# Performance work log

Hardware: AMD Instinct MI355X
Metric: run time of the kernel (lower is better)

The kernel has to match this reference:

```python
import jax, jax.numpy as jnp
import numpy as np

SAMPLE_RATE = 256
WIN = 64          # round(256*250/1000)
HOP = 32          # round(256*125/1000)
HIDDEN = 512
PER_CHAN = 8
MAX_CH = 64
_EEG_BANDS = ((0.5, 4.0), (4.0, 8.0), (8.0, 13.0), (13.0, 30.0), (30.0, 100.0))

_FREQS = np.fft.rfftfreq(WIN, d=1.0 / SAMPLE_RATE)
_BAND_MASKS = [np.logical_and(_FREQS >= lo, _FREQS < hi) for (lo, hi) in _EEG_BANDS]


def _sinusoidal_1d(n, dim, dtype=jnp.float32):
    pos = jnp.arange(n, dtype=jnp.float32)[:, None]
    half = dim // 2
    div = jnp.exp(jnp.arange(half, dtype=jnp.float32) * (-np.log(10000.0) / half))
    ang = pos * div[None, :]
    pe = jnp.zeros((n, dim), dtype=jnp.float32)
    pe = pe.at[:, 0::2].set(jnp.sin(ang))
    pe = pe.at[:, 1::2].set(jnp.cos(ang))
    return pe.astype(dtype)


def setup_inputs() -> dict:
    key = jax.random.key(0)
    k = jax.random.split(key, 5)
    B, T, C = 8, 65536, 64
    return {
        "signal": jax.random.normal(k[0], (B, T, C), dtype=jnp.float32),
        "chan_w": 0.02 * jax.random.normal(k[1], (MAX_CH, 7, PER_CHAN), dtype=jnp.float32),
        "chan_b": 0.02 * jax.random.normal(k[2], (MAX_CH, PER_CHAN), dtype=jnp.float32),
        "mix_w": 0.02 * jax.random.normal(k[3], (HIDDEN, MAX_CH * PER_CHAN), dtype=jnp.float32),
        "marker": 0.02 * jax.random.normal(k[4], (HIDDEN,), dtype=jnp.float32),
    }


def reference(signal, chan_w, chan_b, mix_w, marker):
    B, T, C = signal.shape  # C == MAX_CH, no padding/mask branch
    Tw = (T - WIN) // HOP + 1
    idx = jnp.arange(Tw)[:, None] * HOP + jnp.arange(WIN)[None, :]
    x = jnp.transpose(signal[:, idx, :], (0, 1, 3, 2))
    # spectral features
    mag = jnp.abs(jnp.fft.rfft(x, axis=-1))
    band_feats = jnp.stack(
        [mag[..., m].mean(axis=-1) if m.any() else jnp.zeros(mag.shape[:-1], mag.dtype)
         for m in _BAND_MASKS],
        axis=-1,
    )  # (B, Tw, C, 5)
    mean = x.mean(axis=-1, keepdims=True)
    std = jnp.std(x, axis=-1, ddof=1, keepdims=True)  # torch std is unbiased
    feats = jnp.concatenate([band_feats, mean, std], axis=-1)  # (B, Tw, C, 7)
    # per-channel projection + bias
    emb = jnp.einsum("btcf,cfp->btcp", feats, chan_w) + chan_b[None, None]
    flat = emb.reshape(B, Tw, MAX_CH * PER_CHAN)
    z = flat @ mix_w.T  # (B, Tw, HIDDEN)
    z = z + _sinusoidal_1d(Tw, HIDDEN, z.dtype)[None]
    mk = jnp.broadcast_to(marker[None, None, :], (B, 1, HIDDEN))
    return jnp.concatenate([mk, z], axis=1)  # (B, 1+Tw, HIDDEN)
```

## Files before the change

### kernel.cpp

```cpp
#include <hip/hip_runtime.h>
#include <stdint.h>

#define TW_N 2047
#define BATCH 8
#define T_LEN 65536
#define NCH 64
#define HID 512
#define NWIN (BATCH * TW_N)

typedef unsigned short ushortT;

__device__ __forceinline__ ushortT f2b(float f) {
  union { float f; uint32_t i; } v; v.f = f;
  uint32_t r = v.i + 0x7fffu + ((v.i >> 16) & 1u);
  return (ushortT)(r >> 16);
}
__device__ __forceinline__ uint32_t pk2(float lo, float hi) {
  return (uint32_t)f2b(lo) | ((uint32_t)f2b(hi) << 16);
}

__device__ __forceinline__ void gload_lds16(const void* g, void* l) {
  __builtin_amdgcn_global_load_lds(
      (const __attribute__((address_space(1))) uint32_t*)g,
      (__attribute__((address_space(3))) uint32_t*)l, 16, 0, 0);
}

constexpr float CQ[17] = {
  1.0f, 0.9951847267f, 0.9807852804f, 0.9569403357f, 0.9238795325f,
  0.8819212643f, 0.8314696123f, 0.7730104534f, 0.7071067812f, 0.6343932842f,
  0.5555702330f, 0.4713967368f, 0.3826834324f, 0.2902846773f, 0.1950903220f,
  0.0980171403f, 0.0f };
constexpr float cos64(int m) {
  m &= 63;
  return (m <= 16) ? CQ[m] : (m < 32) ? -CQ[32 - m] : (m < 48) ? -CQ[m - 32] : CQ[64 - m];
}
constexpr float sin64(int m) { return cos64(m - 16); }
struct TwTab { float c[24][32]; float s[24][32]; };
constexpr TwTab make_tab() {
  TwTab t{};
  for (int i = 0; i < 24; ++i)
    for (int j = 0; j < 32; ++j) {
      int m = ((i + 1) * j) & 63;
      t.c[i][j] = cos64(m);
      t.s[i][j] = sin64(m);
    }
  return t;
}
constexpr TwTab TT = make_tab();

__device__ ushortT Bpack[HID * HID];

__global__ __launch_bounds__(256) void prep_kernel(
    const float* __restrict__ marker, const float* __restrict__ Bw,
    float* __restrict__ out)
{
  const int gid = blockIdx.x * 256 + threadIdx.x;
  if (blockIdx.x < 16) {
    out[(size_t)(gid >> 9) * (2048 * 512) + (gid & 511)] = marker[gid & 511];
  } else {
    const int i = (gid - 4096) * 8;
    const float4 f0 = *(const float4*)(Bw + i);
    const float4 f1 = *(const float4*)(Bw + i + 4);
    uint4 u;
    u.x = pk2(f0.x, f0.y); u.y = pk2(f0.z, f0.w);
    u.z = pk2(f1.x, f1.y); u.w = pk2(f1.z, f1.w);
    *(uint4*)(Bpack + i) = u;
  }
}

#define WPB 8
#define SROWS 288

__global__ __launch_bounds__(512) void feat_embed_kernel(
    const float* __restrict__ sig, const float* __restrict__ chw,
    const float* __restrict__ chb, ushortT* __restrict__ flatB)
{
  __shared__ float xs[SROWS * NCH];
  const int tid = threadIdx.x;
  const int tile = blockIdx.x;
  const int b = blockIdx.y;
  const int t0 = tile * (WPB * 32);

  const float* sgb = sig + (size_t)b * T_LEN * NCH;
#pragma unroll
  for (int k = 0; k < 9; ++k) {
    const int idx = tid + k * 512;
    int row = t0 + (idx >> 4);
    row = row < T_LEN ? row : T_LEN - 1;
    gload_lds16(sgb + (size_t)row * NCH + (idx & 15) * 4, (char*)xs + (size_t)idx * 16);
  }
  __syncthreads();

  const int wv = tid >> 6;
  const int c = tid & 63;
  int wl = tile * WPB + wv;
  wl = wl < TW_N ? wl : TW_N - 1;
  const int lv = wl - tile * WPB;
  const float* base = xs + lv * (32 * NCH) + c;

  float e[32], o[32];
  float sum = 0.f, sumsq = 0.f;
#pragma unroll
  for (int t = 0; t < 32; ++t) {
    const float a = base[t * 64];
    const float d = base[(t + 32) * 64];
    e[t] = a + d; o[t] = a - d;
    sum += e[t];
    sumsq = fmaf(a, a, fmaf(d, d, sumsq));
  }

  float b1 = 0.f, b2 = 0.f, b3 = 0.f, b4 = 0.f;
#pragma unroll
  for (int i = 0; i < 24; ++i) {
    const int k = i + 1;
    float re = 0.f, im = 0.f;
#pragma unroll
    for (int t = 0; t < 32; ++t) {
      const float v = (k & 1) ? o[t] : e[t];
      re = fmaf(v, TT.c[i][t], re);
      im = fmaf(v, TT.s[i][t], im);
    }
    const float mag = sqrtf(fmaf(re, re, im * im));
    if (k == 1) b1 += mag;
    else if (k < 4) b2 += mag;
    else if (k < 8) b3 += mag;
    else b4 += mag;
  }

  const float mean = sum * (1.f / 64.f);
  const float var = (sumsq - sum * sum * (1.f / 64.f)) * (1.f / 63.f);
  const float sd = sqrtf(fmaxf(var, 0.f));

  float feats[7];
  feats[0] = 0.f;
  feats[1] = b1;
  feats[2] = b2 * 0.5f;
  feats[3] = b3 * 0.25f;
  feats[4] = b4 * (1.f / 17.f);
  feats[5] = mean;
  feats[6] = sd;

  const float* wr = chw + c * 56;
  float emb[8];
#pragma unroll
  for (int p = 0; p < 8; ++p) emb[p] = chb[c * 8 + p];
#pragma unroll
  for (int f = 1; f < 7; ++f) {
    const float fv = feats[f];
#pragma unroll
    for (int p = 0; p < 8; ++p) emb[p] = fmaf(fv, wr[f * 8 + p], emb[p]);
  }

  uint32_t pka[4];
#pragma unroll
  for (int q = 0; q < 4; ++q) pka[q] = pk2(emb[2 * q], emb[2 * q + 1]);
  const int w = b * TW_N + wl;
  *(uint4*)(flatB + (size_t)w * HID + c * 8) = make_uint4(pka[0], pka[1], pka[2], pka[3]);
}

typedef __attribute__((ext_vector_type(8))) short short8;
typedef __attribute__((ext_vector_type(4))) float f32x4;

__global__ __launch_bounds__(256) void mix_gemm_kernel(
    const ushortT* __restrict__ A,
    float* __restrict__ out)
{
  __shared__ ushortT As[2][128 * 32];
  __shared__ ushortT Bs[2][128 * 32];

  const int tid = threadIdx.x;
  const int lane = tid & 63;
  const int wv = tid >> 6;
  const int wm = wv >> 1, wn = wv & 1;
  const int fr = lane & 15;
  const int fq = lane >> 4;

  const int n0 = blockIdx.x * 128;
  const int m0 = blockIdx.y * 128;

  const int srow = tid >> 2;
  const int sko = (tid & 3) * 8;

  f32x4 acc[4][4];
#pragma unroll
  for (int i = 0; i < 4; ++i)
#pragma unroll
    for (int j = 0; j < 4; ++j) acc[i][j] = (f32x4){0.f, 0.f, 0.f, 0.f};

  int am0 = m0 + srow;       am0 = am0 < NWIN ? am0 : NWIN - 1;
  int am1 = m0 + 64 + srow;  am1 = am1 < NWIN ? am1 : NWIN - 1;
  const ushortT* ga0 = A + (size_t)am0 * HID + sko;
  const ushortT* ga1 = A + (size_t)am1 * HID + sko;
  const ushortT* gb0 = Bpack + (size_t)(n0 + srow) * HID + sko;
  const ushortT* gb1 = Bpack + (size_t)(n0 + 64 + srow) * HID + sko;

#define STAGE(buf, kt) do {                                                    \
    const int ko_ = (kt) * 32;                                                 \
    gload_lds16(ga0 + ko_, (char*)&As[buf][0] + tid * 16);                     \
    gload_lds16(ga1 + ko_, (char*)&As[buf][0] + 4096 + tid * 16);              \
    gload_lds16(gb0 + ko_, (char*)&Bs[buf][0] + tid * 16);                     \
    gload_lds16(gb1 + ko_, (char*)&Bs[buf][0] + 4096 + tid * 16);              \
  } while (0)

  STAGE(0, 0);

  for (int kt = 0; kt < 16; ++kt) {
    const int cur = kt & 1;
    if (kt < 15) {
      STAGE(cur ^ 1, kt + 1);
      asm volatile("s_waitcnt vmcnt(4)\n\ts_barrier" ::: "memory");
    } else {
      asm volatile("s_waitcnt vmcnt(0)\n\ts_barrier" ::: "memory");
    }

    short8 af[4], bf[4];
#pragma unroll
    for (int mt = 0; mt < 4; ++mt)
      af[mt] = *(const short8*)&As[cur][(wm * 64 + mt * 16 + fr) * 32 + fq * 8];
#pragma unroll
    for (int nt = 0; nt < 4; ++nt)
      bf[nt] = *(const short8*)&Bs[cur][(wn * 64 + nt * 16 + fr) * 32 + fq * 8];
#pragma unroll
    for (int mt = 0; mt < 4; ++mt)
#pragma unroll
      for (int nt = 0; nt < 4; ++nt)
        acc[mt][nt] = __builtin_amdgcn_mfma_f32_16x16x32_bf16(af[mt], bf[nt], acc[mt][nt], 0, 0, 0);

    asm volatile("s_barrier" ::: "memory");
  }
#undef STAGE

#pragma unroll
  for (int nt = 0; nt < 4; ++nt) {
    const int ng = n0 + wn * 64 + nt * 16 + fr;
    const float dv = __expf(-0.03597789208f * (float)(ng >> 1));
    const bool odd = (ng & 1);
#pragma unroll
    for (int mt = 0; mt < 4; ++mt) {
#pragma unroll
      for (int r = 0; r < 4; ++r) {
        const int mg = m0 + wm * 64 + mt * 16 + fq * 4 + r;
        if (mg < NWIN) {
          const int bb = mg / TW_N;
          const int tw = mg - bb * TW_N;
          const float ang = (float)tw * dv;
          const float pev = odd ? __cosf(ang) : __sinf(ang);
          out[((size_t)(bb * 2048 + 1 + tw)) * HID + ng] = acc[mt][nt][r] + pev;
        }
      }
    }
  }
}

extern "C" void kernel_launch(void* const* d_in, const int* in_sizes, int n_in,
                              void* d_out, int out_size, void* d_ws, size_t ws_size,
                              hipStream_t stream)
{
  const float* sig = (const float*)d_in[0];
  const float* chw = (const float*)d_in[1];
  const float* chb = (const float*)d_in[2];
  const float* mxw = (const float*)d_in[3];
  const float* mkr = (const float*)d_in[4];
  float* out = (float*)d_out;

  ushortT* flatB = (ushortT*)d_ws;

  hipLaunchKernelGGL(prep_kernel, dim3(144), dim3(256), 0, stream, mkr, mxw, out);
  hipLaunchKernelGGL(feat_embed_kernel, dim3(256, 8), dim3(512), 0, stream, sig, chw, chb, flatB);
  hipLaunchKernelGGL(mix_gemm_kernel, dim3(4, 128), dim3(256), 0, stream, flatB, out);
}
```

Measured before the change: 266.2 us.

## Stream feature windows per wave with register sliding reuse; triple-buffer GEMM LDS

The feature kernel no longer stages signal tiles through LDS. Each wave now handles a run of 8 consecutive windows for one batch and slides a 64-sample window through registers, reusing the overlapping half and loading the next half-window one iteration ahead. This drops the LDS traffic, the barrier and the redundant halo loads, but launches far fewer waves and runs a serial per-wave loop, so latency hiding may suffer. Separately, the mix GEMM moves from double to triple LDS buffering with a deeper vmcnt wait, so global loads are issued two k-steps ahead.

```diff
diff --git a/kernel.cpp b/kernel.cpp
--- a/kernel.cpp
+++ b/kernel.cpp
@@ -68,94 +68,92 @@
   }
 }
 
-#define WPB 8
-#define SROWS 288
-
-__global__ __launch_bounds__(512) void feat_embed_kernel(
+__global__ __launch_bounds__(256) void feat_embed_kernel(
     const float* __restrict__ sig, const float* __restrict__ chw,
     const float* __restrict__ chb, ushortT* __restrict__ flatB)
 {
-  __shared__ float xs[SROWS * NCH];
   const int tid = threadIdx.x;
-  const int tile = blockIdx.x;
-  const int b = blockIdx.y;
-  const int t0 = tile * (WPB * 32);
-
-  const float* sgb = sig + (size_t)b * T_LEN * NCH;
-#pragma unroll
-  for (int k = 0; k < 9; ++k) {
-    const int idx = tid + k * 512;
-    int row = t0 + (idx >> 4);
-    row = row < T_LEN ? row : T_LEN - 1;
-    gload_lds16(sgb + (size_t)row * NCH + (idx & 15) * 4, (char*)xs + (size_t)idx * 16);
-  }
-  __syncthreads();
-
-  const int wv = tid >> 6;
   const int c = tid & 63;
-  int wl = tile * WPB + wv;
-  wl = wl < TW_N ? wl : TW_N - 1;
-  const int lv = wl - tile * WPB;
-  const float* base = xs + lv * (32 * NCH) + c;
-
-  float e[32], o[32];
-  float sum = 0.f, sumsq = 0.f;
-#pragma unroll
-  for (int t = 0; t < 32; ++t) {
-    const float a = base[t * 64];
-    const float d = base[(t + 32) * 64];
-    e[t] = a + d; o[t] = a - d;
-    sum += e[t];
-    sumsq = fmaf(a, a, fmaf(d, d, sumsq));
-  }
-
-  float b1 = 0.f, b2 = 0.f, b3 = 0.f, b4 = 0.f;
-#pragma unroll
-  for (int i = 0; i < 24; ++i) {
-    const int k = i + 1;
-    float re = 0.f, im = 0.f;
+  const int gw = blockIdx.x * 4 + (tid >> 6);
+  const int b = gw >> 8;
+  const int run = gw & 255;
+  const int tw0 = run * 8;
+  const int nw = (tw0 + 8 <= TW_N) ? 8 : (TW_N - tw0);
+  const float* sg = sig + ((size_t)b * T_LEN + (size_t)tw0 * 32) * NCH + c;
+  const float* wr = chw + c * 56;
+
+  float A[32], Bh[32], O[32], R[32];
+#pragma unroll
+  for (int t = 0; t < 32; ++t) A[t] = sg[t * 64];
+#pragma unroll
+  for (int t = 0; t < 32; ++t) Bh[t] = sg[(t + 32) * 64];
+
+#pragma unroll 1
+  for (int l = 0; l < nw; ++l) {
+    {
+      int hrow = (tw0 + l + 2) * 32;
+      hrow = hrow < (T_LEN - 32) ? hrow : (T_LEN - 32);
+      const float* pn = sig + ((size_t)b * T_LEN + hrow) * NCH + c;
+#pragma unroll
+      for (int t = 0; t < 32; ++t) R[t] = pn[t * 64];
+    }
+
+    float sum = 0.f, sumsq = 0.f;
 #pragma unroll
     for (int t = 0; t < 32; ++t) {
-      const float v = (k & 1) ? o[t] : e[t];
-      re = fmaf(v, TT.c[i][t], re);
-      im = fmaf(v, TT.s[i][t], im);
-    }
-    const float mag = sqrtf(fmaf(re, re, im * im));
-    if (k == 1) b1 += mag;
-    else if (k < 4) b2 += mag;
-    else if (k < 8) b3 += mag;
-    else b4 += mag;
-  }
-
-  const float mean = sum * (1.f / 64.f);
-  const float var = (sumsq - sum * sum * (1.f / 64.f)) * (1.f / 63.f);
-  const float sd = sqrtf(fmaxf(var, 0.f));
-
-  float feats[7];
-  feats[0] = 0.f;
-  feats[1] = b1;
-  feats[2] = b2 * 0.5f;
-  feats[3] = b3 * 0.25f;
-  feats[4] = b4 * (1.f / 17.f);
-  feats[5] = mean;
-  feats[6] = sd;
-
-  const float* wr = chw + c * 56;
-  float emb[8];
-#pragma unroll
-  for (int p = 0; p < 8; ++p) emb[p] = chb[c * 8 + p];
-#pragma unroll
-  for (int f = 1; f < 7; ++f) {
-    const float fv = feats[f];
-#pragma unroll
-    for (int p = 0; p < 8; ++p) emb[p] = fmaf(fv, wr[f * 8 + p], emb[p]);
-  }
-
-  uint32_t pka[4];
-#pragma unroll
-  for (int q = 0; q < 4; ++q) pka[q] = pk2(emb[2 * q], emb[2 * q + 1]);
-  const int w = b * TW_N + wl;
-  *(uint4*)(flatB + (size_t)w * HID + c * 8) = make_uint4(pka[0], pka[1], pka[2], pka[3]);
+      O[t] = A[t] - Bh[t];
+      A[t] = A[t] + Bh[t];
+      sum += A[t];
+      sumsq = fmaf(A[t], A[t], fmaf(O[t], O[t], sumsq));
+    }
+
+    float b1 = 0.f, b2 = 0.f, b3 = 0.f, b4 = 0.f;
+#pragma unroll
+    for (int i = 0; i < 24; ++i) {
+      const int k = i + 1;
+      float re = 0.f, im = 0.f;
+#pragma unroll
+      for (int t = 0; t < 32; ++t) {
+        const float v = (k & 1) ? O[t] : A[t];
+        re = fmaf(v, TT.c[i][t], re);
+        im = fmaf(v, TT.s[i][t], im);
+      }
+      const float mag = __builtin_amdgcn_sqrtf(fmaf(re, re, im * im));
+      if (k == 1) b1 += mag;
+      else if (k < 4) b2 += mag;
+      else if (k < 8) b3 += mag;
+      else b4 += mag;
+    }
+
+    const float mean = sum * (1.f / 64.f);
+    const float var = (sumsq * 0.5f - sum * sum * (1.f / 64.f)) * (1.f / 63.f);
+    const float sd = __builtin_amdgcn_sqrtf(fmaxf(var, 0.f));
+
+    const float f1 = b1, f2 = b2 * 0.5f, f3 = b3 * 0.25f, f4 = b4 * (1.f / 17.f);
+    float emb[8];
+#pragma unroll
+    for (int p = 0; p < 8; ++p) emb[p] = chb[c * 8 + p];
+#pragma unroll
+    for (int p = 0; p < 8; ++p) {
+      float e = emb[p];
+      e = fmaf(f1, wr[8 + p], e);
+      e = fmaf(f2, wr[16 + p], e);
+      e = fmaf(f3, wr[24 + p], e);
+      e = fmaf(f4, wr[32 + p], e);
+      e = fmaf(mean, wr[40 + p], e);
+      e = fmaf(sd, wr[48 + p], e);
+      emb[p] = e;
+    }
+
+    uint32_t pka[4];
+#pragma unroll
+    for (int q = 0; q < 4; ++q) pka[q] = pk2(emb[2 * q], emb[2 * q + 1]);
+    const int w = b * TW_N + tw0 + l;
+    *(uint4*)(flatB + (size_t)w * HID + c * 8) = make_uint4(pka[0], pka[1], pka[2], pka[3]);
+
+#pragma unroll
+    for (int t = 0; t < 32; ++t) { A[t] = Bh[t]; Bh[t] = R[t]; }
+  }
 }
 
 typedef __attribute__((ext_vector_type(8))) short short8;
@@ -165,8 +163,8 @@
     const ushortT* __restrict__ A,
     float* __restrict__ out)
 {
-  __shared__ ushortT As[2][128 * 32];
-  __shared__ ushortT Bs[2][128 * 32];
+  __shared__ ushortT As[3][128 * 32];
+  __shared__ ushortT Bs[3][128 * 32];
 
   const int tid = threadIdx.x;
   const int lane = tid & 63;
@@ -203,11 +201,14 @@
   } while (0)
 
   STAGE(0, 0);
-
+  STAGE(1, 1);
+
+  int c0 = 0, c1 = 1, c2 = 2;
   for (int kt = 0; kt < 16; ++kt) {
-    const int cur = kt & 1;
-    if (kt < 15) {
-      STAGE(cur ^ 1, kt + 1);
+    if (kt < 14) {
+      STAGE(c2, kt + 2);
+      asm volatile("s_waitcnt vmcnt(8)\n\ts_barrier" ::: "memory");
+    } else if (kt == 14) {
       asm volatile("s_waitcnt vmcnt(4)\n\ts_barrier" ::: "memory");
     } else {
       asm volatile("s_waitcnt vmcnt(0)\n\ts_barrier" ::: "memory");
@@ -216,10 +217,10 @@
     short8 af[4], bf[4];
 #pragma unroll
     for (int mt = 0; mt < 4; ++mt)
-      af[mt] = *(const short8*)&As[cur][(wm * 64 + mt * 16 + fr) * 32 + fq * 8];
+      af[mt] = *(const short8*)&As[c0][(wm * 64 + mt * 16 + fr) * 32 + fq * 8];
 #pragma unroll
     for (int nt = 0; nt < 4; ++nt)
-      bf[nt] = *(const short8*)&Bs[cur][(wn * 64 + nt * 16 + fr) * 32 + fq * 8];
+      bf[nt] = *(const short8*)&Bs[c0][(wn * 64 + nt * 16 + fr) * 32 + fq * 8];
 #pragma unroll
     for (int mt = 0; mt < 4; ++mt)
 #pragma unroll
@@ -227,6 +228,7 @@
         acc[mt][nt] = __builtin_amdgcn_mfma_f32_16x16x32_bf16(af[mt], bf[nt], acc[mt][nt], 0, 0, 0);
 
     asm volatile("s_barrier" ::: "memory");
+    const int tmp = c0; c0 = c1; c1 = c2; c2 = tmp;
   }
 #undef STAGE
 
@@ -266,6 +268,6 @@
   ushortT* flatB = (ushortT*)d_ws;
 
   hipLaunchKernelGGL(prep_kernel, dim3(144), dim3(256), 0, stream, mkr, mxw, out);
-  hipLaunchKernelGGL(feat_embed_kernel, dim3(256, 8), dim3(512), 0, stream, sig, chw, chb, flatB);
+  hipLaunchKernelGGL(feat_embed_kernel, dim3(512), dim3(256), 0, stream, sig, chw, chb, flatB);
   hipLaunchKernelGGL(mix_gemm_kernel, dim3(4, 128), dim3(256), 0, stream, flatB, out);
 }
```

After: 249.8 us. 1.07x faster.
